# Kernel tuning notes

Hardware: AMD Instinct MI355X
Metric: run time of the kernel (lower is better)

The kernel has to match this reference:

```python
import jax, jax.numpy as jnp
import numpy as np

N_NODES = 20000
N_EDGES = 320000
B, F_IN, H_DIM, P = 4, 16, 64, 12


def _glorot(key, shape):
    fan_in, fan_out = shape[0], shape[-1]
    lim = float(np.sqrt(6.0 / (fan_in + fan_out)))
    return jax.random.uniform(key, shape, jnp.float32, -lim, lim)


def setup_inputs() -> dict:
    key = jax.random.key(0)
    ks = jax.random.split(key, 20)
    x = jax.random.normal(ks[0], (B, N_NODES, F_IN, P), jnp.float32)
    edge_index = jax.random.randint(ks[1], (2, N_EDGES), 0, N_NODES, jnp.int64)
    edge_weight = jax.random.uniform(ks[2], (N_EDGES,), jnp.float32)
    # GCNConv weights (in, out) and biases for z/r/h gates
    Wg_z = _glorot(ks[3], (F_IN, H_DIM)); bg_z = jnp.zeros((H_DIM,), jnp.float32)
    Wg_r = _glorot(ks[4], (F_IN, H_DIM)); bg_r = jnp.zeros((H_DIM,), jnp.float32)
    Wg_h = _glorot(ks[5], (F_IN, H_DIM)); bg_h = jnp.zeros((H_DIM,), jnp.float32)
    # Linear layers on concat([conv_out, H]) -> (2H, H)
    Wl_z = _glorot(ks[6], (2 * H_DIM, H_DIM)); bl_z = jax.random.uniform(ks[7], (H_DIM,), jnp.float32, -0.1, 0.1)
    Wl_r = _glorot(ks[8], (2 * H_DIM, H_DIM)); bl_r = jax.random.uniform(ks[9], (H_DIM,), jnp.float32, -0.1, 0.1)
    Wl_h = _glorot(ks[10], (2 * H_DIM, H_DIM)); bl_h = jax.random.uniform(ks[11], (H_DIM,), jnp.float32, -0.1, 0.1)
    att = jax.random.uniform(ks[12], (P,), jnp.float32)  # attention logits over periods
    W_out = _glorot(ks[13], (H_DIM, P)); b_out = jax.random.uniform(ks[14], (P,), jnp.float32, -0.1, 0.1)
    return {"x": x, "edge_index": edge_index, "edge_weight": edge_weight,
            "Wg_z": Wg_z, "bg_z": bg_z, "Wg_r": Wg_r, "bg_r": bg_r, "Wg_h": Wg_h, "bg_h": bg_h,
            "Wl_z": Wl_z, "bl_z": bl_z, "Wl_r": Wl_r, "bl_r": bl_r, "Wl_h": Wl_h, "bl_h": bl_h,
            "att": att, "W_out": W_out, "b_out": b_out}


def reference(x, edge_index, edge_weight, Wg_z, bg_z, Wg_r, bg_r, Wg_h, bg_h,
              Wl_z, bl_z, Wl_r, bl_r, Wl_h, bl_h, att, W_out, b_out):
    Bsz, N, F, Pn = x.shape
    Hh = Wg_z.shape[1]
    # --- gcn_norm: add self loops (weight 1.0), D^-1/2 (A+I) D^-1/2 ---
    loop = jnp.arange(N)
    src = jnp.concatenate([edge_index[0], loop])
    dst = jnp.concatenate([edge_index[1], loop])
    w = jnp.concatenate([edge_weight, jnp.ones((N,), x.dtype)])
    deg = jnp.zeros((N,), x.dtype).at[dst].add(w)
    dinv = jnp.where(deg > 0, jax.lax.rsqrt(deg), 0.0)
    norm = dinv[src] * w * dinv[dst]  # (E+N,)
    # --- propagate raw features once for all periods: (A_hat X) W == A_hat (X W) ---
    xf = x.reshape(Bsz, N, F * Pn)
    msg = xf[:, src, :] * norm[None, :, None]            # (B, E+N, F*P) gather
    agg = jnp.zeros((Bsz, N, F * Pn), x.dtype).at[:, dst, :].add(msg)  # scatter-add
    agg = agg.reshape(Bsz, N, F, Pn)
    # --- A3TGCN2: per-period single GRU step from H=0, attention-pooled ---
    probs = jax.nn.softmax(att)
    H0 = jnp.zeros((Bsz, N, Hh), x.dtype)

    def step(acc, inp):
        a, p = inp  # a: (B, N, F) aggregated features of this period
        cz = a @ Wg_z + bg_z
        cr = a @ Wg_r + bg_r
        ch = a @ Wg_h + bg_h
        Z = jax.nn.sigmoid(jnp.concatenate([cz, H0], -1) @ Wl_z + bl_z)
        R = jax.nn.sigmoid(jnp.concatenate([cr, H0], -1) @ Wl_r + bl_r)
        Ht = jnp.tanh(jnp.concatenate([ch, H0 * R], -1) @ Wl_h + bl_h)
        Hn = Z * H0 + (1.0 - Z) * Ht
        return acc + p * Hn, None

    a_seq = jnp.moveaxis(agg, -1, 0)  # (P, B, N, F)
    Hacc, _ = jax.lax.scan(step, H0, (a_seq, probs))
    # --- trailing ReLU + Linear ---
    return jax.nn.relu(Hacc) @ W_out + b_out  # (B, N, P)
```

## Files before the change

kernel.cpp:

```cpp
#include <hip/hip_runtime.h>
#include <cstdint>
#include <cstddef>

#define NN 20000
#define NE 320000
#define NB 4
#define NF 16
#define NH 64
#define NP 12
#define FP (NF*NP)
#define ROWB (FP*2)
#define NROWB (NB*ROWB)
#define GRID_MAIN 2000

typedef _Float16 h2_t __attribute__((ext_vector_type(2)));
typedef _Float16 h4_t __attribute__((ext_vector_type(4)));
typedef float    f4_t __attribute__((ext_vector_type(4)));

union U32H2 { unsigned u; h2_t h; };
union U64H4 { uint2 u; h4_t h; };

__global__ __launch_bounds__(256) void k_pre1(const float* __restrict__ x,
                                              _Float16* __restrict__ xh,
                                              const int* __restrict__ ei,
                                              const float* __restrict__ ew,
                                              float* deg, int* counts) {
    int blk = blockIdx.x;
    if (blk < 3750) {
        int i = blk * 256 + threadIdx.x;
        int n = i / 48;
        int c = i - n * 48;
        const float4* xf = (const float4*)x;
        h4_t* xo = (h4_t*)xh;
#pragma unroll
        for (int b = 0; b < NB; ++b) {
            float4 v = xf[(size_t)b * (NN * 48) + i];
            h4_t o = { (_Float16)v.x, (_Float16)v.y, (_Float16)v.z, (_Float16)v.w };
            xo[(n * NB + b) * 48 + c] = o;
        }
    } else {
        int e = (blk - 3750) * 256 + threadIdx.x;
        int dst = ei[NE + e];
        atomicAdd(&deg[dst], ew[e]);
        atomicAdd(&counts[dst], 1);
    }
}

__global__ __launch_bounds__(1024) void k_prep(
        const float* __restrict__ deg, float* __restrict__ dinv,
        const int* __restrict__ counts, int* __restrict__ offsets, int* gbase,
        const float* __restrict__ Wg_z, const float* __restrict__ bg_z,
        const float* __restrict__ Wg_h, const float* __restrict__ bg_h,
        const float* __restrict__ Wl_z, const float* __restrict__ bl_z,
        const float* __restrict__ Wl_h, const float* __restrict__ bl_h,
        const float* __restrict__ att, const float* __restrict__ W_out,
        uint2* __restrict__ wfrag, uint2* __restrict__ wofrag,
        float* bz_eff, float* bh_eff, float* probs) {
    int blk = blockIdx.x;
    int t = threadIdx.x;
    if (blk < 20) {
        __shared__ int sums[1024];
        __shared__ int base_sh;
        int i = blk * 1000 + t;
        int slots = 0;
        if (t < 1000) {
            dinv[i] = rsqrtf(1.0f + deg[i]);
            slots = counts[i] + 1;
        }
        sums[t] = slots;
        __syncthreads();
        for (int off = 1; off < 1024; off <<= 1) {
            int v = (t >= off) ? sums[t - off] : 0;
            __syncthreads();
            sums[t] += v;
            __syncthreads();
        }
        if (t == 1023) base_sh = atomicAdd(gbase, sums[1023]);
        __syncthreads();
        if (t < 1000) offsets[i] = base_sh + sums[t] - slots;
        return;
    }
    __shared__ float wzl[NF][NH + 1];
    __shared__ float whl[NF][NH + 1];
    {
        int f = t >> 6, j = t & 63;
        float sz = 0.f, sh = 0.f;
        for (int k = 0; k < NH; ++k) {
            sz += Wg_z[f * NH + k] * Wl_z[k * NH + j];
            sh += Wg_h[f * NH + k] * Wl_h[k * NH + j];
        }
        wzl[f][j] = sz;
        whl[f][j] = sh;
    }
    if (t < NH) {
        float bz = bl_z[t], bh = bl_h[t];
        for (int k = 0; k < NH; ++k) {
            bz += bg_z[k] * Wl_z[k * NH + t];
            bh += bg_h[k] * Wl_h[k * NH + t];
        }
        bz_eff[t] = bz;
        bh_eff[t] = bh;
    }
    if (t == 0) {
        float m = att[0];
        for (int p = 1; p < NP; ++p) m = fmaxf(m, att[p]);
        float s = 0.f, e_[NP];
        for (int p = 0; p < NP; ++p) { e_[p] = expf(att[p] - m); s += e_[p]; }
        for (int p = 0; p < 16; ++p) probs[p] = (p < NP) ? e_[p] / s : 0.f;
    }
    __syncthreads();
    if (t < 512) {
        int ln = t & 63, c = (t >> 6) & 3, zh = t >> 8;
        int kb = 4 * (ln >> 4);
        int j  = 16 * c + (ln & 15);
        float v0, v1, v2, v3;
        if (zh == 0) { v0 = wzl[kb][j]; v1 = wzl[kb+1][j]; v2 = wzl[kb+2][j]; v3 = wzl[kb+3][j]; }
        else         { v0 = whl[kb][j]; v1 = whl[kb+1][j]; v2 = whl[kb+2][j]; v3 = whl[kb+3][j]; }
        union { _Float16 h[4]; uint2 u; } pk;
        pk.h[0] = (_Float16)v0; pk.h[1] = (_Float16)v1;
        pk.h[2] = (_Float16)v2; pk.h[3] = (_Float16)v3;
        wfrag[(zh * 4 + c) * 64 + ln] = pk.u;
    }
    if (t < 256) {
        int ln = t & 63, s = t >> 6;
        int kj = 16 * s + 4 * (ln >> 4);
        int nn_ = ln & 15;
        union { _Float16 h[4]; uint2 u; } pk;
        for (int i = 0; i < 4; ++i)
            pk.h[i] = (_Float16)((nn_ < NP) ? W_out[(kj + i) * NP + nn_] : 0.f);
        wofrag[s * 64 + ln] = pk.u;
    }
}

__global__ __launch_bounds__(256) void k_fill(const int* __restrict__ ei,
                                              const float* __restrict__ ew,
                                              const float* __restrict__ dinv,
                                              const int* __restrict__ offsets,
                                              const int* __restrict__ counts,
                                              int* cursor, uint2* __restrict__ erec) {
    int e = blockIdx.x * 256 + threadIdx.x;
    if (e < NE) {
        int s = ei[e];
        int d = ei[NE + e];
        float nm = dinv[s] * ew[e] * dinv[d];
        int pos = atomicAdd(&cursor[d], 1);
        int idx = offsets[d] + pos;
        _Float16 hn = (_Float16)nm;
        U32H2 w; w.h = (h2_t){hn, hn};
        erec[idx] = make_uint2((unsigned)(s * NROWB), w.u);
    } else if (e < NE + NN) {
        int node = e - NE;
        float di = dinv[node];
        _Float16 hn = (_Float16)(di * di);
        U32H2 w; w.h = (h2_t){hn, hn};
        erec[offsets[node] + counts[node]] = make_uint2((unsigned)(node * NROWB), w.u);
    }
}

__global__ __launch_bounds__(256) void k_main(
        const _Float16* __restrict__ xh,
        const int* __restrict__ offsets, const int* __restrict__ counts,
        const uint2* __restrict__ erec,
        const uint2* __restrict__ wfrag, const uint2* __restrict__ wofrag,
        const float* __restrict__ bz_eff, const float* __restrict__ bh_eff,
        const float* __restrict__ probs, const float* __restrict__ b_out,
        float* __restrict__ out) {
    __shared__ _Float16 a_lds[NB][FP];
    __shared__ _Float16 r_lds[2][NB][NH + 8];
    __shared__ uint2    wz_lds[512];
    __shared__ uint2    wo_lds[256];
    __shared__ float    bzh_lds[128];
    __shared__ float    pr_lds[16];
    __shared__ float    bo_lds[12];

    int t = threadIdx.x;
    wz_lds[t]       = wfrag[t];
    wz_lds[t + 256] = wfrag[t + 256];
    wo_lds[t]       = wofrag[t];
    if (t < 128) bzh_lds[t] = (t < 64) ? bz_eff[t] : bh_eff[t - 64];
    if (t < 16)  pr_lds[t] = probs[t];
    if (t < 12)  bo_lds[t] = b_out[t];
    __syncthreads();

    int b = t >> 6;
    int lane = t & 63;
    int half = lane >> 5;
    int g = lane >> 4, p = lane & 15;

    const char* xbase = (const char*)xh;
    int lb = b * ROWB + (lane & 31) * 12;

    int it = 0;
    for (int n = blockIdx.x; n < NN; n += GRID_MAIN, ++it) {
        int beg = offsets[n];
        int last = beg + counts[n];
        int end = last + 1;

        h2_t A0 = {(_Float16)0.f, (_Float16)0.f};
        h2_t A1 = A0, A2 = A0;

        uint2 qa0, qa1, qa2, qa3, qa4, qa5, qa6, qa7;
        {
            int e0 = beg;
#define LQ(K, QV) { int s_ = e0 + 2*(K) + half; int i_ = s_ < last ? s_ : last; QV = erec[i_]; }
            LQ(0,qa0) LQ(1,qa1) LQ(2,qa2) LQ(3,qa3) LQ(4,qa4) LQ(5,qa5) LQ(6,qa6) LQ(7,qa7)
#undef LQ
        }

        int ecur = beg;
        while (true) {
            int enext = ecur + 16;
            bool more = enext < end;
            uint2 qb0, qb1, qb2, qb3, qb4, qb5, qb6, qb7;
            if (more) {
#define LQ(K, QV) { int s_ = enext + 2*(K) + half; int i_ = s_ < last ? s_ : last; QV = erec[i_]; }
                LQ(0,qb0) LQ(1,qb1) LQ(2,qb2) LQ(3,qb3) LQ(4,qb4) LQ(5,qb5) LQ(6,qb6) LQ(7,qb7)
#undef LQ
            }
            uint3 u0 = *(const uint3*)(xbase + qa0.x + lb);
            uint3 u1 = *(const uint3*)(xbase + qa1.x + lb);
            uint3 u2 = *(const uint3*)(xbase + qa2.x + lb);
            uint3 u3 = *(const uint3*)(xbase + qa3.x + lb);
            uint3 u4 = *(const uint3*)(xbase + qa4.x + lb);
            uint3 u5 = *(const uint3*)(xbase + qa5.x + lb);
            uint3 u6 = *(const uint3*)(xbase + qa6.x + lb);
            uint3 u7 = *(const uint3*)(xbase + qa7.x + lb);
#define ACC(K, QV, UV) { \
                int s_ = ecur + 2*(K) + half; \
                unsigned w_ = (s_ <= last) ? QV.y : 0u; \
                U32H2 wu; wu.u = w_; \
                U32H2 x0; x0.u = UV.x; U32H2 x1; x1.u = UV.y; U32H2 x2; x2.u = UV.z; \
                A0 += wu.h * x0.h; A1 += wu.h * x1.h; A2 += wu.h * x2.h; }
            ACC(0,qa0,u0) ACC(1,qa1,u1) ACC(2,qa2,u2) ACC(3,qa3,u3)
            ACC(4,qa4,u4) ACC(5,qa5,u5) ACC(6,qa6,u6) ACC(7,qa7,u7)
#undef ACC
            if (!more) break;
            qa0=qb0; qa1=qb1; qa2=qb2; qa3=qb3; qa4=qb4; qa5=qb5; qa6=qb6; qa7=qb7;
            ecur = enext;
        }

        {
            U32H2 t0, t1, t2, s0, s1, s2;
            t0.h = A0; t1.h = A1; t2.h = A2;
            s0.u = (unsigned)__shfl_xor((int)t0.u, 32, 64);
            s1.u = (unsigned)__shfl_xor((int)t1.u, 32, 64);
            s2.u = (unsigned)__shfl_xor((int)t2.u, 32, 64);
            A0 += s0.h; A1 += s1.h; A2 += s2.h;
        }

        if (lane < 32) {
            unsigned* aw = (unsigned*)&a_lds[b][0];
            U32H2 t0, t1, t2; t0.h = A0; t1.h = A1; t2.h = A2;
            int L = lane;
            aw[3 * L + 0] = t0.u;
            aw[3 * L + 1] = t1.u;
            aw[3 * L + 2] = t2.u;
        }

        int pe = (p < NP) ? p : 0;
        const _Float16* ab = &a_lds[b][48 * g + pe];
        h4_t A = { ab[0], ab[12], ab[24], ab[36] };

        f4_t accz[4], acch[4];
#pragma unroll
        for (int c = 0; c < 4; ++c) {
            float bzv = bzh_lds[16 * c + p];
            float bhv = bzh_lds[64 + 16 * c + p];
            accz[c] = (f4_t){bzv, bzv, bzv, bzv};
            acch[c] = (f4_t){bhv, bhv, bhv, bhv};
        }
#pragma unroll
        for (int c = 0; c < 4; ++c) {
            U64H4 fz; fz.u = wz_lds[c * 64 + lane];
            U64H4 fh; fh.u = wz_lds[(4 + c) * 64 + lane];
            accz[c] = __builtin_amdgcn_mfma_f32_16x16x16f16(A, fz.h, accz[c], 0, 0, 0);
            acch[c] = __builtin_amdgcn_mfma_f32_16x16x16f16(A, fh.h, acch[c], 0, 0, 0);
        }

#pragma unroll
        for (int c = 0; c < 4; ++c) {
            float partial = 0.f;
#pragma unroll
            for (int r = 0; r < 4; ++r) {
                float zz = accz[c][r];
                float hh = acch[c][r];
                float sn = __builtin_amdgcn_rcpf(1.f + __expf(zz));
                float th = 1.f - 2.f * __builtin_amdgcn_rcpf(__expf(2.f * hh) + 1.f);
                partial = fmaf(pr_lds[4 * g + r], sn * th, partial);
            }
            partial += __shfl_xor(partial, 16, 64);
            partial += __shfl_xor(partial, 32, 64);
            if (g == 0) r_lds[it & 1][b][16 * c + p] = (_Float16)fmaxf(partial, 0.f);
        }
        __syncthreads();

        if (t < 64) {
            float bo = bo_lds[p < NP ? p : 0];
            f4_t co = (f4_t){bo, bo, bo, bo};
            int pb = p & 3;
#pragma unroll
            for (int s = 0; s < 4; ++s) {
                h4_t Ao = *(const h4_t*)&r_lds[it & 1][pb][16 * s + 4 * g];
                U64H4 Bo; Bo.u = wo_lds[s * 64 + lane];
                co = __builtin_amdgcn_mfma_f32_16x16x16f16(Ao, Bo.h, co, 0, 0, 0);
            }
            if (g == 0 && p < NP) {
                size_t baseo = (size_t)n * NP + p;
#pragma unroll
                for (int r = 0; r < 4; ++r)
                    out[(size_t)r * ((size_t)NN * NP) + baseo] = co[r];
            }
        }
    }
}


extern "C" void kernel_launch(void* const* d_in, const int* in_sizes, int n_in,
                              void* d_out, int out_size, void* d_ws, size_t ws_size,
                              hipStream_t stream) {
    const float* x     = (const float*)d_in[0];
    const int*   ei    = (const int*)d_in[1];
    const float* ew    = (const float*)d_in[2];
    const float* Wg_z  = (const float*)d_in[3];
    const float* bg_z  = (const float*)d_in[4];
    const float* Wg_h  = (const float*)d_in[7];
    const float* bg_h  = (const float*)d_in[8];
    const float* Wl_z  = (const float*)d_in[9];
    const float* bl_z  = (const float*)d_in[10];
    const float* Wl_h  = (const float*)d_in[13];
    const float* bl_h  = (const float*)d_in[14];
    const float* att   = (const float*)d_in[15];
    const float* W_out = (const float*)d_in[16];
    const float* b_out = (const float*)d_in[17];
    float*       out   = (float*)d_out;

    char* p = (char*)d_ws;
    auto alloc = [&](size_t bytes) -> void* {
        void* r = (void*)p;
        p += (bytes + 255) & ~(size_t)255;
        return r;
    };
    const size_t PAD_NN = ((size_t)NN * 4 + 255) & ~(size_t)255;
    float*     deg     = (float*)alloc(NN * 4);
    int*       counts  = (int*)  alloc(NN * 4);
    int*       cursor  = (int*)  alloc(NN * 4);
    int*       gbase   = (int*)  alloc(256);
    float*     dinv    = (float*)alloc(NN * 4);
    int*       offsets = (int*)  alloc(NN * 4);
    uint2*     erec    = (uint2*)alloc((size_t)(NE + NN) * 8);
    uint2*     wfrag   = (uint2*)alloc(512 * 8);
    uint2*     wofrag  = (uint2*)alloc(256 * 8);
    float*     bz_eff  = (float*)alloc(NH * 4);
    float*     bh_eff  = (float*)alloc(NH * 4);
    float*     probs   = (float*)alloc(16 * 4);
    _Float16*  xh      = (_Float16*)alloc((size_t)NN * NROWB);

    hipMemsetAsync(deg, 0, PAD_NN * 3 + 256, stream);

    k_pre1 <<<5000, 256, 0, stream>>>(x, xh, ei, ew, deg, counts);
    k_prep <<<21, 1024, 0, stream>>>(deg, dinv, counts, offsets, gbase,
                                     Wg_z, bg_z, Wg_h, bg_h, Wl_z, bl_z, Wl_h, bl_h,
                                     att, W_out, wfrag, wofrag, bz_eff, bh_eff, probs);
    k_fill <<<(NE + NN + 255) / 256, 256, 0, stream>>>(ei, ew, dinv, offsets, counts, cursor, erec);
    k_main <<<GRID_MAIN, 256, 0, stream>>>(xh, offsets, counts, erec,
                                           wfrag, wofrag, bz_eff, bh_eff, probs, b_out, out);
}
```

Before: 176.5 us.

## Split output projection into separate batched MFMA kernel via fp16 hidden buffer

The per-node output linear layer, which ran on a single wave after a block-wide barrier inside the main loop, is moved into a new kernel. The main kernel now writes the ReLU'd pooled hidden state (fp16) to a global buffer, and k_out runs dense 16-row MFMA tiles over all batch-node rows. This removes the idle three-wave tail and the LDS staging of the output weights from the gather kernel. In exchange it adds an extra launch and a global round trip of the hidden buffer, and a barrier is still kept before the MFMA stage to protect a_lds reuse.

Measured after the change: 179.8 us. About the same (+1.9%).

```diff
diff --git a/kernel.cpp b/kernel.cpp
--- a/kernel.cpp
+++ b/kernel.cpp
@@ -160,26 +160,19 @@
 __global__ __launch_bounds__(256) void k_main(
         const _Float16* __restrict__ xh,
         const int* __restrict__ offsets, const int* __restrict__ counts,
-        const uint2* __restrict__ erec,
-        const uint2* __restrict__ wfrag, const uint2* __restrict__ wofrag,
+        const uint2* __restrict__ erec, const uint2* __restrict__ wfrag,
         const float* __restrict__ bz_eff, const float* __restrict__ bh_eff,
-        const float* __restrict__ probs, const float* __restrict__ b_out,
-        float* __restrict__ out) {
+        const float* __restrict__ probs, _Float16* __restrict__ rout) {
     __shared__ _Float16 a_lds[NB][FP];
-    __shared__ _Float16 r_lds[2][NB][NH + 8];
     __shared__ uint2    wz_lds[512];
-    __shared__ uint2    wo_lds[256];
     __shared__ float    bzh_lds[128];
     __shared__ float    pr_lds[16];
-    __shared__ float    bo_lds[12];
 
     int t = threadIdx.x;
     wz_lds[t]       = wfrag[t];
     wz_lds[t + 256] = wfrag[t + 256];
-    wo_lds[t]       = wofrag[t];
     if (t < 128) bzh_lds[t] = (t < 64) ? bz_eff[t] : bh_eff[t - 64];
     if (t < 16)  pr_lds[t] = probs[t];
-    if (t < 12)  bo_lds[t] = b_out[t];
     __syncthreads();
 
     int b = t >> 6;
@@ -190,8 +183,7 @@
     const char* xbase = (const char*)xh;
     int lb = b * ROWB + (lane & 31) * 12;
 
-    int it = 0;
-    for (int n = blockIdx.x; n < NN; n += GRID_MAIN, ++it) {
+    for (int n = blockIdx.x; n < NN; n += GRID_MAIN) {
         int beg = offsets[n];
         int last = beg + counts[n];
         int end = last + 1;
@@ -261,6 +253,8 @@
         const _Float16* ab = &a_lds[b][48 * g + pe];
         h4_t A = { ab[0], ab[12], ab[24], ab[36] };
 
+        __syncthreads();
+
         f4_t accz[4], acch[4];
 #pragma unroll
         for (int c = 0; c < 4; ++c) {
@@ -277,6 +271,7 @@
             acch[c] = __builtin_amdgcn_mfma_f32_16x16x16f16(A, fh.h, acch[c], 0, 0, 0);
         }
 
+        float rh0, rh1, rh2, rh3;
 #pragma unroll
         for (int c = 0; c < 4; ++c) {
             float partial = 0.f;
@@ -290,27 +285,37 @@
             }
             partial += __shfl_xor(partial, 16, 64);
             partial += __shfl_xor(partial, 32, 64);
-            if (g == 0) r_lds[it & 1][b][16 * c + p] = (_Float16)fmaxf(partial, 0.f);
-        }
-        __syncthreads();
-
-        if (t < 64) {
-            float bo = bo_lds[p < NP ? p : 0];
-            f4_t co = (f4_t){bo, bo, bo, bo};
-            int pb = p & 3;
-#pragma unroll
-            for (int s = 0; s < 4; ++s) {
-                h4_t Ao = *(const h4_t*)&r_lds[it & 1][pb][16 * s + 4 * g];
-                U64H4 Bo; Bo.u = wo_lds[s * 64 + lane];
-                co = __builtin_amdgcn_mfma_f32_16x16x16f16(Ao, Bo.h, co, 0, 0, 0);
-            }
-            if (g == 0 && p < NP) {
-                size_t baseo = (size_t)n * NP + p;
-#pragma unroll
-                for (int r = 0; r < 4; ++r)
-                    out[(size_t)r * ((size_t)NN * NP) + baseo] = co[r];
-            }
-        }
+            float v = fmaxf(partial, 0.f);
+            if (c == 0) rh0 = v; else if (c == 1) rh1 = v; else if (c == 2) rh2 = v; else rh3 = v;
+        }
+        float r01 = (g & 1) ? rh1 : rh0;
+        float r23 = (g & 1) ? rh3 : rh2;
+        float rsel = (g & 2) ? r23 : r01;
+        rout[((size_t)b * NN + n) * NH + lane] = (_Float16)rsel;
+    }
+}
+
+__global__ __launch_bounds__(256) void k_out(
+        const _Float16* __restrict__ rout, const uint2* __restrict__ wofrag,
+        const float* __restrict__ b_out, float* __restrict__ out) {
+    int lane = threadIdx.x & 63;
+    int g = lane >> 4, p = lane & 15;
+    int tile = blockIdx.x * 4 + (threadIdx.x >> 6);
+    int u0 = tile * 16;
+
+    float bo = b_out[p < NP ? p : 0];
+    f4_t co = (f4_t){bo, bo, bo, bo};
+    const h4_t* arow = (const h4_t*)(rout + (size_t)(u0 + p) * NH);
+#pragma unroll
+    for (int s = 0; s < 4; ++s) {
+        h4_t Ao = arow[4 * s + g];
+        U64H4 Bo; Bo.u = wofrag[s * 64 + lane];
+        co = __builtin_amdgcn_mfma_f32_16x16x16f16(Ao, Bo.h, co, 0, 0, 0);
+    }
+    if (p < NP) {
+#pragma unroll
+        for (int r = 0; r < 4; ++r)
+            out[(size_t)(u0 + 4 * g + r) * NP + p] = co[r];
     }
 }
 
@@ -354,6 +359,7 @@
     float*     bh_eff  = (float*)alloc(NH * 4);
     float*     probs   = (float*)alloc(16 * 4);
     _Float16*  xh      = (_Float16*)alloc((size_t)NN * NROWB);
+    _Float16*  rout    = (_Float16*)alloc((size_t)NN * NB * NH * 2);
 
     hipMemsetAsync(deg, 0, PAD_NN * 3 + 256, stream);
 
@@ -362,6 +368,7 @@
                                      Wg_z, bg_z, Wg_h, bg_h, Wl_z, bl_z, Wl_h, bl_h,
                                      att, W_out, wfrag, wofrag, bz_eff, bh_eff, probs);
     k_fill <<<(NE + NN + 255) / 256, 256, 0, stream>>>(ei, ew, dinv, offsets, counts, cursor, erec);
-    k_main <<<GRID_MAIN, 256, 0, stream>>>(xh, offsets, counts, erec,
-                                           wfrag, wofrag, bz_eff, bh_eff, probs, b_out, out);
-}
+    k_main <<<GRID_MAIN, 256, 0, stream>>>(xh, offsets, counts, erec, wfrag,
+                                           bz_eff, bh_eff, probs, rout);
+    k_out  <<<1250, 256, 0, stream>>>(rout, wofrag, b_out, out);
+}
```
